# Kernel tuning notes

Hardware: AMD Instinct MI355X
Metric: run time of the kernel (lower is better)

Reference implementation:

```python
import jax, jax.numpy as jnp
import numpy as np

BN_EPS = 1e-5

def _bn(x, g, b):
    # BatchNorm1d, training-mode batch statistics
    mu = x.mean(axis=0)
    var = x.var(axis=0)
    return g * (x - mu) / jnp.sqrt(var + BN_EPS) + b

def setup_inputs() -> dict:
    key = jax.random.key(0)
    ks = jax.random.split(key, 10)
    B2, D_in, D1, DIMS, C = 16384, 1024, 512, 256, 40
    B = B2 // 2
    def w(k, shape, fan_in):
        return jax.random.normal(k, shape, jnp.float32) / np.float32(np.sqrt(fan_in))
    return {
        "lufeat": jax.random.normal(ks[0], (B2, D_in), jnp.float32),
        "llabel": jax.random.randint(ks[1], (B,), 0, C),
        "W1": w(ks[2], (D_in, D1), D_in), "b1": jnp.zeros(D1, jnp.float32),
        "W2": w(ks[3], (D1, DIMS), D1), "b2": jnp.zeros(DIMS, jnp.float32),
        "W3": w(ks[4], (DIMS + C, 256), DIMS + C), "b3": jnp.zeros(256, jnp.float32),
        "W4": w(ks[5], (256, 64), 256), "b4": jnp.zeros(64, jnp.float32),
        "W5": w(ks[6], (64, 1), 64), "b5": jnp.zeros(1, jnp.float32),
        "g1": jnp.ones(256, jnp.float32), "be1": jnp.zeros(256, jnp.float32),
        "g2": jnp.ones(64, jnp.float32), "be2": jnp.zeros(64, jnp.float32),
        "mbank0": jax.random.normal(ks[7], (C, DIMS), jnp.float32),
        "start0": jnp.zeros(C, jnp.float32),
    }

def reference(lufeat, llabel, W1, b1, W2, b2, W3, b3, W4, b4, W5, b5,
              g1, be1, g2, be2, mbank0, start0):
    B = lufeat.shape[0] // 2
    h = (lufeat @ W1 + b1) @ W2 + b2            # [2B, dims]
    h = h / jnp.linalg.norm(h, axis=1, keepdims=True)
    lfeat, ufeat = h[:B], h[B:]

    # Sequential per-sample memory-bank scatter/EMA update (detached feats)
    lf_sg = jax.lax.stop_gradient(lfeat)
    def step(carry, xs):
        start, mbank = carry
        lab, feat = xs
        row = jnp.where(start[lab] == 0, feat, 0.9 * mbank[lab] + 0.1 * feat)
        return (start.at[lab].set(1.0), mbank.at[lab].set(row)), None
    (_, mbank), _ = jax.lax.scan(step, (start0, mbank0), (llabel, lf_sg))
    mbank = jax.lax.stop_gradient(mbank)

    # cdist retrieval: [B, C] euclidean distances
    lm = jnp.linalg.norm(lfeat[:, None, :] - mbank[None, :, :], axis=-1)
    lscores = lm.min(axis=-1)
    um = jnp.linalg.norm(ufeat[:, None, :] - mbank[None, :, :], axis=-1)

    uf = jnp.concatenate([ufeat, um], axis=-1)   # [B, dims + C]
    u = jax.nn.relu(_bn(uf @ W3 + b3, g1, be1))
    u = jax.nn.relu(_bn(u @ W4 + b4, g2, be2))   # dropout = identity (eval)
    uscores = u @ W5 + b5                        # [B, 1]
    return lscores, uscores, mbank
```

## Files before the change

kernel.cpp:

```cpp
#include <hip/hip_runtime.h>
#include <hip/hip_bf16.h>
#include <stdint.h>

typedef __attribute__((ext_vector_type(4))) float f32x4;
typedef __attribute__((ext_vector_type(8))) short s16x8;
typedef __attribute__((ext_vector_type(4))) unsigned short u16x4;
typedef __attribute__((ext_vector_type(4))) int i32x4;

#define B2T 16384
#define BH 8192
#define DIN 1024
#define DD1 512
#define DIMS 256
#define NC 40
#define CAPS 2048

__device__ __forceinline__ unsigned short f2b(float f) {
  unsigned int u = __builtin_bit_cast(unsigned int, f);
  u += 0x7FFFu + ((u >> 16) & 1u);
  return (unsigned short)(u >> 16);
}

__global__ __launch_bounds__(256) void prep_all(const float* __restrict__ W1,
                                                const float* __restrict__ W2,
                                                const float* __restrict__ b1,
                                                const float* __restrict__ b2,
                                                const float* __restrict__ W3,
                                                const float* __restrict__ W4,
                                                unsigned short* __restrict__ WeffT,
                                                float* __restrict__ beff,
                                                unsigned short* __restrict__ W3T,
                                                unsigned short* __restrict__ W4T,
                                                float* __restrict__ statz) {
  __shared__ float W1s[32][36];
  __shared__ float W2sT[32][36];
  int b = blockIdx.x, t = threadIdx.x;
  if (b < 256) {
    int k0 = (b & 31) * 32, n0 = (b >> 5) * 32;
    int nn = t & 31, kq = t >> 5;
    f32x4 acc = (f32x4){0.f, 0.f, 0.f, 0.f};
    for (int j0 = 0; j0 < DD1; j0 += 32) {
#pragma unroll
      for (int i = 0; i < 4; ++i) {
        int idx = t + 256 * i;
        int kk = idx >> 5, jj = idx & 31;
        W1s[kk][jj] = W1[(size_t)(k0 + kk) * DD1 + j0 + jj];
        W2sT[jj][kk] = W2[(size_t)(j0 + kk) * DIMS + n0 + jj];
      }
      __syncthreads();
#pragma unroll
      for (int jj4 = 0; jj4 < 8; ++jj4) {
        f32x4 w2 = *(const f32x4*)&W2sT[nn][jj4 * 4];
        f32x4 w1_0 = *(const f32x4*)&W1s[kq * 4 + 0][jj4 * 4];
        f32x4 w1_1 = *(const f32x4*)&W1s[kq * 4 + 1][jj4 * 4];
        f32x4 w1_2 = *(const f32x4*)&W1s[kq * 4 + 2][jj4 * 4];
        f32x4 w1_3 = *(const f32x4*)&W1s[kq * 4 + 3][jj4 * 4];
        acc[0] += w1_0[0] * w2[0] + w1_0[1] * w2[1] + w1_0[2] * w2[2] + w1_0[3] * w2[3];
        acc[1] += w1_1[0] * w2[0] + w1_1[1] * w2[1] + w1_1[2] * w2[2] + w1_1[3] * w2[3];
        acc[2] += w1_2[0] * w2[0] + w1_2[1] * w2[1] + w1_2[2] * w2[2] + w1_2[3] * w2[3];
        acc[3] += w1_3[0] * w2[0] + w1_3[1] * w2[1] + w1_3[2] * w2[2] + w1_3[3] * w2[3];
      }
      __syncthreads();
    }
    u16x4 pk = {f2b(acc[0]), f2b(acc[1]), f2b(acc[2]), f2b(acc[3])};
    *(u16x4*)(WeffT + (size_t)(n0 + nn) * DIN + k0 + kq * 4) = pk;
  } else if (b == 256) {
    float a0 = 0.f, a1 = 0.f, a2 = 0.f, a3 = 0.f, a4 = 0.f, a5 = 0.f, a6 = 0.f, a7 = 0.f;
    for (int j = 0; j < DD1; j += 8) {
      a0 += b1[j + 0] * W2[(size_t)(j + 0) * DIMS + t];
      a1 += b1[j + 1] * W2[(size_t)(j + 1) * DIMS + t];
      a2 += b1[j + 2] * W2[(size_t)(j + 2) * DIMS + t];
      a3 += b1[j + 3] * W2[(size_t)(j + 3) * DIMS + t];
      a4 += b1[j + 4] * W2[(size_t)(j + 4) * DIMS + t];
      a5 += b1[j + 5] * W2[(size_t)(j + 5) * DIMS + t];
      a6 += b1[j + 6] * W2[(size_t)(j + 6) * DIMS + t];
      a7 += b1[j + 7] * W2[(size_t)(j + 7) * DIMS + t];
    }
    beff[t] = b2[t] + (((a0 + a1) + (a2 + a3)) + ((a4 + a5) + (a6 + a7)));
  } else if (b < 577) {
    int idx = (b - 257) * 256 + t;
    int n = idx / 320, k = idx - n * 320;
    float v = (k < 296) ? W3[(size_t)k * 256 + n] : 0.0f;
    W3T[(size_t)n * 320 + k] = f2b(v);
  } else if (b < 641) {
    int idx = (b - 577) * 256 + t;
    int n = idx >> 8, k = idx & 255;
    W4T[(size_t)n * 256 + k] = f2b(W4[(size_t)k * 64 + n]);
  } else {
    for (int i = t; i < 640; i += 256) statz[i] = 0.0f;
  }
}

template <int AMODE, int NB, int MI, int CW, int EPI>
__global__ __launch_bounds__(256) void gemm_core(
    const void* __restrict__ Aptr, int lda, const unsigned short* __restrict__ BT,
    const float* __restrict__ bias, float* __restrict__ C, int ldc, int K,
    float* __restrict__ sums, float* __restrict__ ssqs,
    const float* __restrict__ bnsum, const float* __restrict__ bnssq,
    const float* __restrict__ bng, const float* __restrict__ bnbe,
    unsigned short* __restrict__ uf) {
  constexpr int AR = (4 / CW) * MI * 16;
  constexpr int ABN = AR / 32;
  constexpr int BBN = NB * 8 / 256;
  __shared__ short A_s[AR][72];
  __shared__ short B_s[NB][72];
  __shared__ float rs[4][AR];
  int t = threadIdx.x;
  int m0 = blockIdx.x * AR;
  int w = t >> 6, lane = t & 63, q = lane >> 4, ln = lane & 15;
  f32x4 acc[MI][4];
#pragma unroll
  for (int mi = 0; mi < MI; ++mi)
#pragma unroll
    for (int ni = 0; ni < 4; ++ni) acc[mi][ni] = (f32x4){0.f, 0.f, 0.f, 0.f};

  f32x4 pa[ABN][2];
  s16x8 pab[ABN];
  s16x8 pb[BBN];

#pragma unroll
  for (int i = 0; i < ABN; ++i) {
    int ch = t + 256 * i, row = ch >> 3, kp = (ch & 7) * 8;
    if constexpr (AMODE == 1) {
      const unsigned short* A = (const unsigned short*)Aptr;
      pab[i] = *(const s16x8*)(A + (size_t)(m0 + row) * lda + kp);
    } else {
      const float* A = (const float*)Aptr;
      const f32x4* src = (const f32x4*)(A + (size_t)(m0 + row) * lda + kp);
      pa[i][0] = src[0];
      pa[i][1] = src[1];
    }
  }
#pragma unroll
  for (int i = 0; i < BBN; ++i) {
    int ch = t + 256 * i, n = ch >> 3, kp = (ch & 7) * 8;
    pb[i] = *(const s16x8*)(BT + (size_t)n * K + kp);
  }

  for (int kk = 0; kk < K; kk += 64) {
#pragma unroll
    for (int i = 0; i < ABN; ++i) {
      int ch = t + 256 * i, row = ch >> 3, kp = (ch & 7) * 8;
      if constexpr (AMODE == 1) {
        *(s16x8*)&A_s[row][kp] = pab[i];
      } else {
        f32x4 v0 = pa[i][0], v1 = pa[i][1];
        if constexpr (AMODE == 2) {
          float vv[8] = {v0[0], v0[1], v0[2], v0[3], v1[0], v1[1], v1[2], v1[3]};
#pragma unroll
          for (int j = 0; j < 8; ++j) {
            int f = kk + kp + j;
            float mu = bnsum[f] * (1.0f / 8192.0f);
            float var = bnssq[f] * (1.0f / 8192.0f) - mu * mu;
            float sc = bng[f] * rsqrtf(var + 1e-5f);
            float sh = bnbe[f] - mu * sc;
            vv[j] = fmaxf(vv[j] * sc + sh, 0.0f);
          }
          v0 = (f32x4){vv[0], vv[1], vv[2], vv[3]};
          v1 = (f32x4){vv[4], vv[5], vv[6], vv[7]};
        }
        s16x8 p;
        p[0] = (short)f2b(v0[0]); p[1] = (short)f2b(v0[1]);
        p[2] = (short)f2b(v0[2]); p[3] = (short)f2b(v0[3]);
        p[4] = (short)f2b(v1[0]); p[5] = (short)f2b(v1[1]);
        p[6] = (short)f2b(v1[2]); p[7] = (short)f2b(v1[3]);
        *(s16x8*)&A_s[row][kp] = p;
      }
    }
#pragma unroll
    for (int i = 0; i < BBN; ++i) {
      int ch = t + 256 * i, n = ch >> 3, kp = (ch & 7) * 8;
      *(s16x8*)&B_s[n][kp] = pb[i];
    }
    __syncthreads();

    if (kk + 64 < K) {
      int kn = kk + 64;
#pragma unroll
      for (int i = 0; i < ABN; ++i) {
        int ch = t + 256 * i, row = ch >> 3, kp = (ch & 7) * 8;
        if constexpr (AMODE == 1) {
          const unsigned short* A = (const unsigned short*)Aptr;
          pab[i] = *(const s16x8*)(A + (size_t)(m0 + row) * lda + kn + kp);
        } else {
          const float* A = (const float*)Aptr;
          const f32x4* src = (const f32x4*)(A + (size_t)(m0 + row) * lda + kn + kp);
          pa[i][0] = src[0];
          pa[i][1] = src[1];
        }
      }
#pragma unroll
      for (int i = 0; i < BBN; ++i) {
        int ch = t + 256 * i, n = ch >> 3, kp = (ch & 7) * 8;
        pb[i] = *(const s16x8*)(BT + (size_t)n * K + kn + kp);
      }
    }

#pragma unroll
    for (int k32 = 0; k32 < 64; k32 += 32) {
      s16x8 af[MI];
      int ab = (w / CW) * MI * 16;
#pragma unroll
      for (int mi = 0; mi < MI; ++mi)
        af[mi] = *(const s16x8*)&A_s[ab + mi * 16 + ln][k32 + q * 8];
      int nb0 = (w % CW) * 64;
#pragma unroll
      for (int ni = 0; ni < 4; ++ni) {
        s16x8 bfr = *(const s16x8*)&B_s[nb0 + ni * 16 + ln][k32 + q * 8];
#pragma unroll
        for (int mi = 0; mi < MI; ++mi)
          acc[mi][ni] = __builtin_amdgcn_mfma_f32_16x16x32_bf16(af[mi], bfr, acc[mi][ni], 0, 0, 0);
      }
    }
    __syncthreads();
  }

  float v[MI][4][4];
#pragma unroll
  for (int mi = 0; mi < MI; ++mi)
#pragma unroll
    for (int ni = 0; ni < 4; ++ni) {
      float bv = bias[(w % CW) * 64 + ni * 16 + ln];
#pragma unroll
      for (int r = 0; r < 4; ++r) v[mi][ni][r] = acc[mi][ni][r] + bv;
    }

  if constexpr (EPI == 1) {
    float p[MI][4];
#pragma unroll
    for (int mi = 0; mi < MI; ++mi)
#pragma unroll
      for (int r = 0; r < 4; ++r) {
        float s = v[mi][0][r] * v[mi][0][r] + v[mi][1][r] * v[mi][1][r] +
                  v[mi][2][r] * v[mi][2][r] + v[mi][3][r] * v[mi][3][r];
        s += __shfl_xor(s, 1); s += __shfl_xor(s, 2);
        s += __shfl_xor(s, 4); s += __shfl_xor(s, 8);
        p[mi][r] = s;
      }
    if (ln == 0) {
#pragma unroll
      for (int mi = 0; mi < MI; ++mi)
#pragma unroll
        for (int r = 0; r < 4; ++r) rs[w][mi * 16 + q * 4 + r] = p[mi][r];
    }
    __syncthreads();
    if (t < AR) rs[0][t] = rsqrtf(rs[0][t] + rs[1][t] + rs[2][t] + rs[3][t]);
    __syncthreads();
#pragma unroll
    for (int mi = 0; mi < MI; ++mi)
#pragma unroll
      for (int r = 0; r < 4; ++r) {
        int rib = mi * 16 + q * 4 + r;
        float inv = rs[0][rib];
        int grow = m0 + rib;
#pragma unroll
        for (int ni = 0; ni < 4; ++ni) {
          int col = w * 64 + ni * 16 + ln;
          float nv = v[mi][ni][r] * inv;
          C[(size_t)grow * ldc + col] = nv;
          if (grow >= BH) uf[(size_t)(grow - BH) * 320 + col] = f2b(nv);
        }
      }
  } else {
#pragma unroll
    for (int mi = 0; mi < MI; ++mi)
#pragma unroll
      for (int ni = 0; ni < 4; ++ni)
#pragma unroll
        for (int r = 0; r < 4; ++r) {
          int grow = m0 + (w / CW) * MI * 16 + mi * 16 + q * 4 + r;
          int col = (w % CW) * 64 + ni * 16 + ln;
          C[(size_t)grow * ldc + col] = v[mi][ni][r];
        }
    if constexpr (EPI == 2 || EPI == 3) {
#pragma unroll
      for (int ni = 0; ni < 4; ++ni) {
        float s = 0.f, s2 = 0.f;
#pragma unroll
        for (int mi = 0; mi < MI; ++mi)
#pragma unroll
          for (int r = 0; r < 4; ++r) {
            float x = v[mi][ni][r];
            s += x; s2 += x * x;
          }
        s += __shfl_xor(s, 16); s += __shfl_xor(s, 32);
        s2 += __shfl_xor(s2, 16); s2 += __shfl_xor(s2, 32);
        if (q == 0) {
          int col = (w % CW) * 64 + ni * 16 + ln;
          atomicAdd(&sums[col], s);
          atomicAdd(&ssqs[col], s2);
        }
      }
    }
  }
}

__global__ __launch_bounds__(256) void bank_kernel(const int* __restrict__ llabel,
                                                   const float* __restrict__ Hn,
                                                   const float* __restrict__ mbank0,
                                                   const float* __restrict__ start0,
                                                   float* __restrict__ mbank_out,
                                                   float* __restrict__ msq) {
  __shared__ i32x4 lab4[BH / 4];
  __shared__ int idx_s[CAPS];
  __shared__ int wcnt[4];
  __shared__ float red[4];
  int t = threadIdx.x, c = blockIdx.x;
  int w = t >> 6, lane = t & 63;

  for (int i = t; i < BH / 4; i += 256) lab4[i] = ((const i32x4*)llabel)[i];
  __syncthreads();
  const int* lab_s = (const int*)lab4;

  int base0 = w * (BH / 4);
  int cnt = 0;
  for (int b = 0; b < BH / 4; b += 64)
    cnt += (int)__popcll(__ballot(lab_s[base0 + b + lane] == c));
  if (lane == 0) wcnt[w] = cnt;
  __syncthreads();
  int off = 0;
#pragma unroll
  for (int i = 0; i < 4; ++i)
    if (i < w) off += wcnt[i];
  int Ktot = wcnt[0] + wcnt[1] + wcnt[2] + wcnt[3];

  int running = off;
  for (int b = 0; b < BH / 4; b += 64) {
    bool hit = lab_s[base0 + b + lane] == c;
    unsigned long long mk = __ballot(hit);
    if (hit) {
      int pos = running + (int)__popcll(mk & ((1ull << lane) - 1ull));
      if (pos < CAPS) idx_s[pos] = base0 + b + lane;
    }
    running += (int)__popcll(mk);
  }
  __syncthreads();
  int K = Ktot < CAPS ? Ktot : CAPS;

  const float l09 = -0.15200309344504997f;
  bool fresh = (start0[c] == 0.0f);
  float out;
  if (K == 0) {
    out = mbank0[(size_t)c * DIMS + t];
  } else {
    float a0 = 0.f, a1 = 0.f, a2 = 0.f, a3 = 0.f, a4 = 0.f, a5 = 0.f, a6 = 0.f, a7 = 0.f;
    float w0fold = fresh ? exp2f((float)K * l09) : 0.f;
    int m = 0;
    for (; m + 8 <= K; m += 8) {
      float e = (float)(K - 1 - m);
      float wa = 0.1f * exp2f(e * l09) + (m == 0 ? w0fold : 0.f);
      a0 += wa * Hn[(size_t)idx_s[m + 0] * DIMS + t];
      a1 += 0.1f * exp2f((e - 1.f) * l09) * Hn[(size_t)idx_s[m + 1] * DIMS + t];
      a2 += 0.1f * exp2f((e - 2.f) * l09) * Hn[(size_t)idx_s[m + 2] * DIMS + t];
      a3 += 0.1f * exp2f((e - 3.f) * l09) * Hn[(size_t)idx_s[m + 3] * DIMS + t];
      a4 += 0.1f * exp2f((e - 4.f) * l09) * Hn[(size_t)idx_s[m + 4] * DIMS + t];
      a5 += 0.1f * exp2f((e - 5.f) * l09) * Hn[(size_t)idx_s[m + 5] * DIMS + t];
      a6 += 0.1f * exp2f((e - 6.f) * l09) * Hn[(size_t)idx_s[m + 6] * DIMS + t];
      a7 += 0.1f * exp2f((e - 7.f) * l09) * Hn[(size_t)idx_s[m + 7] * DIMS + t];
    }
    for (; m < K; ++m) {
      float wa = 0.1f * exp2f((float)(K - 1 - m) * l09) + (m == 0 ? w0fold : 0.f);
      a0 += wa * Hn[(size_t)idx_s[m] * DIMS + t];
    }
    float acc = ((a0 + a1) + (a2 + a3)) + ((a4 + a5) + (a6 + a7));
    float base_v = fresh ? 0.f : exp2f((float)K * l09) * mbank0[(size_t)c * DIMS + t];
    out = acc + base_v;
  }
  mbank_out[(size_t)c * DIMS + t] = out;
  float vv = out * out;
#pragma unroll
  for (int o = 32; o; o >>= 1) vv += __shfl_xor(vv, o);
  if ((t & 63) == 0) red[t >> 6] = vv;
  __syncthreads();
  if (t == 0) msq[c] = (red[0] + red[1]) + (red[2] + red[3]);
}

__global__ __launch_bounds__(256) void dist_kernel(const float* __restrict__ Hn,
                                                   const float* __restrict__ mbank,
                                                   const float* __restrict__ msq,
                                                   float* __restrict__ lscores,
                                                   unsigned short* __restrict__ uf) {
  __shared__ float Ms[NC][260];
  __shared__ float Hs[32][260];
  __shared__ float msq_s[NC];
  int t = threadIdx.x;
  int r0 = blockIdx.x * 32;
  for (int e = t; e < NC * 256; e += 256) {
    int i = e >> 8, d = e & 255;
    Ms[i][d] = mbank[(size_t)i * DIMS + d];
  }
  for (int e = t; e < 32 * 256; e += 256) {
    int i = e >> 8, d = e & 255;
    Hs[i][d] = Hn[(size_t)(r0 + i) * DIMS + d];
  }
  if (t < NC) msq_s[t] = msq[t];
  __syncthreads();
  int r = t >> 3, c0 = (t & 7) * 5;
  float g0 = 0, g1 = 0, g2 = 0, g3 = 0, g4 = 0;
  for (int d = 0; d < DIMS; d += 4) {
    f32x4 f = *(const f32x4*)&Hs[r][d];
    f32x4 m0v = *(const f32x4*)&Ms[c0 + 0][d];
    f32x4 m1v = *(const f32x4*)&Ms[c0 + 1][d];
    f32x4 m2v = *(const f32x4*)&Ms[c0 + 2][d];
    f32x4 m3v = *(const f32x4*)&Ms[c0 + 3][d];
    f32x4 m4v = *(const f32x4*)&Ms[c0 + 4][d];
    g0 += f[0] * m0v[0] + f[1] * m0v[1] + f[2] * m0v[2] + f[3] * m0v[3];
    g1 += f[0] * m1v[0] + f[1] * m1v[1] + f[2] * m1v[2] + f[3] * m1v[3];
    g2 += f[0] * m2v[0] + f[1] * m2v[1] + f[2] * m2v[2] + f[3] * m2v[3];
    g3 += f[0] * m3v[0] + f[1] * m3v[1] + f[2] * m3v[2] + f[3] * m3v[3];
    g4 += f[0] * m4v[0] + f[1] * m4v[1] + f[2] * m4v[2] + f[3] * m4v[3];
  }
  int row = r0 + r;
  float d2[5];
  d2[0] = 1.0f + msq_s[c0 + 0] - 2.0f * g0;
  d2[1] = 1.0f + msq_s[c0 + 1] - 2.0f * g1;
  d2[2] = 1.0f + msq_s[c0 + 2] - 2.0f * g2;
  d2[3] = 1.0f + msq_s[c0 + 3] - 2.0f * g3;
  d2[4] = 1.0f + msq_s[c0 + 4] - 2.0f * g4;
  if (row < BH) {
    float mn = fminf(fminf(fminf(d2[0], d2[1]), fminf(d2[2], d2[3])), d2[4]);
    mn = fminf(mn, __shfl_xor(mn, 1, 8));
    mn = fminf(mn, __shfl_xor(mn, 2, 8));
    mn = fminf(mn, __shfl_xor(mn, 4, 8));
    if ((t & 7) == 0) lscores[row] = sqrtf(fmaxf(mn, 0.0f));
  } else {
    unsigned short* dst = uf + (size_t)(row - BH) * 320 + 256 + c0;
#pragma unroll
    for (int qq = 0; qq < 5; ++qq) dst[qq] = f2b(sqrtf(fmaxf(d2[qq], 0.0f)));
  }
}

__global__ __launch_bounds__(256) void uscore_bn(const float* __restrict__ y2,
                                                 const float* __restrict__ sums2,
                                                 const float* __restrict__ ssqs2,
                                                 const float* __restrict__ g2,
                                                 const float* __restrict__ be2,
                                                 const float* __restrict__ W5,
                                                 const float* __restrict__ b5,
                                                 float* __restrict__ out) {
  int t = threadIdx.x;
  int wv = t >> 6, lane = t & 63;
  int row = blockIdx.x * 4 + wv;
  float mu = sums2[lane] * (1.0f / 8192.0f);
  float var = ssqs2[lane] * (1.0f / 8192.0f) - mu * mu;
  float sc = g2[lane] * rsqrtf(var + 1e-5f);
  float sh = be2[lane] - mu * sc;
  float v = fmaxf(y2[(size_t)row * 64 + lane] * sc + sh, 0.0f) * W5[lane];
#pragma unroll
  for (int o = 32; o; o >>= 1) v += __shfl_xor(v, o);
  if (lane == 0) out[row] = v + b5[0];
}

extern "C" void kernel_launch(void* const* d_in, const int* in_sizes, int n_in,
                              void* d_out, int out_size, void* d_ws, size_t ws_size,
                              hipStream_t stream) {
  const float* lufeat = (const float*)d_in[0];
  const int* llabel = (const int*)d_in[1];
  const float* W1 = (const float*)d_in[2];
  const float* b1 = (const float*)d_in[3];
  const float* W2 = (const float*)d_in[4];
  const float* b2 = (const float*)d_in[5];
  const float* W3 = (const float*)d_in[6];
  const float* b3 = (const float*)d_in[7];
  const float* W4 = (const float*)d_in[8];
  const float* b4 = (const float*)d_in[9];
  const float* W5 = (const float*)d_in[10];
  const float* b5 = (const float*)d_in[11];
  const float* g1 = (const float*)d_in[12];
  const float* be1 = (const float*)d_in[13];
  const float* g2 = (const float*)d_in[14];
  const float* be2 = (const float*)d_in[15];
  const float* mbank0 = (const float*)d_in[16];
  const float* start0 = (const float*)d_in[17];

  char* ws = (char*)d_ws;
  unsigned short* WeffT = (unsigned short*)(ws + 0);
  float* Hraw = (float*)(ws + 524288);
  float* ybuf = (float*)(ws + 524288);
  float* y2 = (float*)(ws + 8912896);
  unsigned short* uf = (unsigned short*)(ws + 17301504);
  unsigned short* W3T = (unsigned short*)(ws + 22544384);
  unsigned short* W4T = (unsigned short*)(ws + 22708224);
  float* beff = (float*)(ws + 22740992);
  float* sums1 = (float*)(ws + 22742016);
  float* ssq1 = sums1 + 256;
  float* sums2 = ssq1 + 256;
  float* ssq2 = sums2 + 64;
  float* msq = (float*)(ws + 22744576);

  float* lscores = (float*)d_out;
  float* uscores = lscores + 8192;
  float* mbank = uscores + 8192;

  prep_all<<<642, 256, 0, stream>>>(W1, W2, b1, b2, W3, W4, WeffT, beff, W3T, W4T, sums1);
  gemm_core<0, 256, 2, 4, 1><<<512, 256, 0, stream>>>(
      lufeat, 1024, WeffT, beff, Hraw, 256, 1024,
      nullptr, nullptr, nullptr, nullptr, nullptr, nullptr, uf);
  bank_kernel<<<NC, 256, 0, stream>>>(llabel, Hraw, mbank0, start0, mbank, msq);
  dist_kernel<<<512, 256, 0, stream>>>(Hraw, mbank, msq, lscores, uf);
  gemm_core<1, 256, 2, 4, 2><<<256, 256, 0, stream>>>(
      uf, 320, W3T, b3, ybuf, 256, 320,
      sums1, ssq1, nullptr, nullptr, nullptr, nullptr, nullptr);
  gemm_core<2, 64, 1, 1, 3><<<128, 256, 0, stream>>>(
      ybuf, 256, W4T, b4, y2, 64, 256,
      sums2, ssq2, sums1, ssq1, g1, be1, nullptr);
  uscore_bn<<<2048, 256, 0, stream>>>(y2, sums2, ssq2, g2, be2, W5, b5, uscores);
}
```

Before: 239.4 us.

## Double-buffer GEMM register prefetch and precompute BN scale/shift in shared memory

```diff
diff --git a/kernel.cpp b/kernel.cpp
--- a/kernel.cpp
+++ b/kernel.cpp
@@ -105,6 +105,8 @@
   __shared__ short A_s[AR][72];
   __shared__ short B_s[NB][72];
   __shared__ float rs[4][AR];
+  __shared__ float bsc_s[(AMODE == 2) ? 256 : 1];
+  __shared__ float bsh_s[(AMODE == 2) ? 256 : 1];
   int t = threadIdx.x;
   int m0 = blockIdx.x * AR;
   int w = t >> 6, lane = t & 63, q = lane >> 4, ln = lane & 15;
@@ -114,47 +116,60 @@
 #pragma unroll
     for (int ni = 0; ni < 4; ++ni) acc[mi][ni] = (f32x4){0.f, 0.f, 0.f, 0.f};
 
-  f32x4 pa[ABN][2];
-  s16x8 pab[ABN];
-  s16x8 pb[BBN];
-
-#pragma unroll
-  for (int i = 0; i < ABN; ++i) {
-    int ch = t + 256 * i, row = ch >> 3, kp = (ch & 7) * 8;
-    if constexpr (AMODE == 1) {
-      const unsigned short* A = (const unsigned short*)Aptr;
-      pab[i] = *(const s16x8*)(A + (size_t)(m0 + row) * lda + kp);
-    } else {
-      const float* A = (const float*)Aptr;
-      const f32x4* src = (const f32x4*)(A + (size_t)(m0 + row) * lda + kp);
-      pa[i][0] = src[0];
-      pa[i][1] = src[1];
-    }
-  }
-#pragma unroll
-  for (int i = 0; i < BBN; ++i) {
-    int ch = t + 256 * i, n = ch >> 3, kp = (ch & 7) * 8;
-    pb[i] = *(const s16x8*)(BT + (size_t)n * K + kp);
-  }
-
-  for (int kk = 0; kk < K; kk += 64) {
+  f32x4 pa[2][ABN][2];
+  s16x8 pab[2][ABN];
+  s16x8 pb[2][BBN];
+
+  auto issue_loads = [&](int kbase, int buf) {
 #pragma unroll
     for (int i = 0; i < ABN; ++i) {
       int ch = t + 256 * i, row = ch >> 3, kp = (ch & 7) * 8;
       if constexpr (AMODE == 1) {
-        *(s16x8*)&A_s[row][kp] = pab[i];
+        const unsigned short* A = (const unsigned short*)Aptr;
+        pab[buf][i] = *(const s16x8*)(A + (size_t)(m0 + row) * lda + kbase + kp);
       } else {
-        f32x4 v0 = pa[i][0], v1 = pa[i][1];
+        const float* A = (const float*)Aptr;
+        const f32x4* src = (const f32x4*)(A + (size_t)(m0 + row) * lda + kbase + kp);
+        pa[buf][i][0] = src[0];
+        pa[buf][i][1] = src[1];
+      }
+    }
+#pragma unroll
+    for (int i = 0; i < BBN; ++i) {
+      int ch = t + 256 * i, n = ch >> 3, kp = (ch & 7) * 8;
+      pb[buf][i] = *(const s16x8*)(BT + (size_t)n * K + kbase + kp);
+    }
+  };
+
+  if constexpr (AMODE == 2) {
+    float mu = bnsum[t] * (1.0f / 8192.0f);
+    float var = bnssq[t] * (1.0f / 8192.0f) - mu * mu;
+    float sc = bng[t] * rsqrtf(var + 1e-5f);
+    bsc_s[t] = sc;
+    bsh_s[t] = bnbe[t] - mu * sc;
+    __syncthreads();
+  }
+
+  const int nst = K >> 6;
+  issue_loads(0, 0);
+  if (nst > 1) issue_loads(64, 1);
+
+  for (int s = 0; s < nst; ++s) {
+    int kk = s << 6;
+    int buf = s & 1;
+#pragma unroll
+    for (int i = 0; i < ABN; ++i) {
+      int ch = t + 256 * i, row = ch >> 3, kp = (ch & 7) * 8;
+      if constexpr (AMODE == 1) {
+        *(s16x8*)&A_s[row][kp] = pab[buf][i];
+      } else {
+        f32x4 v0 = pa[buf][i][0], v1 = pa[buf][i][1];
         if constexpr (AMODE == 2) {
           float vv[8] = {v0[0], v0[1], v0[2], v0[3], v1[0], v1[1], v1[2], v1[3]};
 #pragma unroll
           for (int j = 0; j < 8; ++j) {
             int f = kk + kp + j;
-            float mu = bnsum[f] * (1.0f / 8192.0f);
-            float var = bnssq[f] * (1.0f / 8192.0f) - mu * mu;
-            float sc = bng[f] * rsqrtf(var + 1e-5f);
-            float sh = bnbe[f] - mu * sc;
-            vv[j] = fmaxf(vv[j] * sc + sh, 0.0f);
+            vv[j] = fmaxf(vv[j] * bsc_s[f] + bsh_s[f], 0.0f);
           }
           v0 = (f32x4){vv[0], vv[1], vv[2], vv[3]};
           v1 = (f32x4){vv[4], vv[5], vv[6], vv[7]};
@@ -170,31 +185,11 @@
 #pragma unroll
     for (int i = 0; i < BBN; ++i) {
       int ch = t + 256 * i, n = ch >> 3, kp = (ch & 7) * 8;
-      *(s16x8*)&B_s[n][kp] = pb[i];
+      *(s16x8*)&B_s[n][kp] = pb[buf][i];
     }
     __syncthreads();
 
-    if (kk + 64 < K) {
-      int kn = kk + 64;
-#pragma unroll
-      for (int i = 0; i < ABN; ++i) {
-        int ch = t + 256 * i, row = ch >> 3, kp = (ch & 7) * 8;
-        if constexpr (AMODE == 1) {
-          const unsigned short* A = (const unsigned short*)Aptr;
-          pab[i] = *(const s16x8*)(A + (size_t)(m0 + row) * lda + kn + kp);
-        } else {
-          const float* A = (const float*)Aptr;
-          const f32x4* src = (const f32x4*)(A + (size_t)(m0 + row) * lda + kn + kp);
-          pa[i][0] = src[0];
-          pa[i][1] = src[1];
-        }
-      }
-#pragma unroll
-      for (int i = 0; i < BBN; ++i) {
-        int ch = t + 256 * i, n = ch >> 3, kp = (ch & 7) * 8;
-        pb[i] = *(const s16x8*)(BT + (size_t)n * K + kn + kp);
-      }
-    }
+    if (s + 2 < nst) issue_loads(kk + 128, buf);
 
 #pragma unroll
     for (int k32 = 0; k32 < 64; k32 += 32) {
```

New measurement: 359.6 us. 1.5x slower.
